# Performance work log

Measured on AMD Instinct MI355X. Metric: run time of the kernel, lower is better.

The kernel has to match this reference:

```python
import jax, jax.numpy as jnp
import numpy as np

N = 8192
IN_F = 256
HEADS = 4
HF = 64            # head_features = out_features / heads
OUT_F = HEADS * HF # concat=True
NEG_SLOPE = 0.2


def setup_inputs() -> dict:
    key = jax.random.key(0)
    ks = jax.random.split(key, 7)
    x = jax.random.normal(ks[0], (N, IN_F), dtype=jnp.float32)
    graph = jax.random.randint(ks[1], (N, N), 0, 2, dtype=jnp.int32)
    weight = jax.random.normal(ks[2], (HEADS, IN_F, HF), dtype=jnp.float32) * (1.0 / np.sqrt(IN_F))
    weight_i = jax.random.normal(ks[3], (HEADS, HF, 1), dtype=jnp.float32) * (1.0 / np.sqrt(HF))
    weight_j = jax.random.normal(ks[4], (HEADS, HF, 1), dtype=jnp.float32) * (1.0 / np.sqrt(HF))
    weight_r = jax.random.normal(ks[5], (IN_F, HF * HEADS), dtype=jnp.float32) * (1.0 / np.sqrt(IN_F))
    bias = jnp.zeros((OUT_F,), dtype=jnp.float32)
    return {"x": x, "graph": graph, "weight": weight, "weight_i": weight_i,
            "weight_j": weight_j, "weight_r": weight_r, "bias": bias}


def reference(x, graph, weight, weight_i, weight_j, weight_r, bias):
    # h: per-head projected features [heads, N, hf]
    h = jnp.einsum('nm,hmf->hnf', x, weight)
    # additive attention logits: coe_i [h,N,1] + coe_j [h,1,N]
    coe_i = jnp.einsum('hnf,hfo->hno', h, weight_i)          # [heads, N, 1]
    coe_j = jnp.einsum('hnf,hfo->hno', h, weight_j)          # [heads, N, 1]
    coe = jax.nn.leaky_relu(coe_i + jnp.swapaxes(coe_j, 1, 2), NEG_SLOPE)  # [heads, N, N]
    # adjacency mask (note transpose, matching the torch code)
    mask = jnp.where(graph > 0, 0.0, -jnp.inf).T             # [N, N]
    att = jax.nn.softmax(coe + mask[None], axis=-1)          # [heads, N, N]
    # aggregate and move heads to axis 1: [N, heads, hf]
    y = jnp.einsum('hij,hjf->ihf', att, h)
    # residual with projection (in_features != head_features)
    y = y + (x @ weight_r).reshape(N, HEADS, HF)
    # concat heads + bias
    y = y.reshape(N, OUT_F) + bias
    return y
```

## Files before the change

### kernel.cpp

```cpp
#include <hip/hip_runtime.h>
#include <hip/hip_bf16.h>

#define N 8192
#define IN_F 256
#define HEADS 4
#define HF 64
#define OUT_F 256

typedef __attribute__((ext_vector_type(8))) short short8;
typedef __attribute__((ext_vector_type(4))) float f32x4;

__device__ __forceinline__ float lrelu(float x) {
    return fmaxf(x, 0.0f) * 0.8f + x * 0.2f;
}
__device__ __forceinline__ short f2bf(float f) {
    union { __hip_bfloat16 h; short s; } u;
    u.h = __float2bfloat16(f);
    return u.s;
}
__device__ __forceinline__ float bf2f(unsigned short b) {
    union { unsigned u; float f; } v; v.u = ((unsigned)b) << 16;
    return v.f;
}
__device__ __forceinline__ unsigned pack_bf16(float p0, float p1) {
    union { __hip_bfloat162 b; unsigned u; } cv;
    cv.b = __float22bfloat162_rn(make_float2(p0, p1));
    return cv.u;
}

__global__ __launch_bounds__(256) void k_wcvt(
    const float* __restrict__ w, const float* __restrict__ wr,
    unsigned short* __restrict__ BbT)
{
    int c = blockIdx.x;
    int k = threadIdx.x;
    float v;
    if (c < 256) {
        int head = c >> 6, f = c & 63;
        v = w[((size_t)head * IN_F + k) * HF + f];
    } else {
        v = wr[(size_t)k * OUT_F + (c - 256)];
    }
    BbT[(size_t)c * IN_F + k] = (unsigned short)f2bf(v);
}

__global__ __launch_bounds__(256) void k_gemm(
    const float* __restrict__ x, const unsigned short* __restrict__ BbT,
    const float* __restrict__ bias,
    unsigned short* __restrict__ hT, float* __restrict__ out)
{
    __shared__ unsigned short Asw[64 * 64];
    __shared__ unsigned short Bsw[128 * 64];
    int t = threadIdx.x;
    int m0 = blockIdx.x * 64;
    int bn = blockIdx.y;
    int w_ = t >> 6, l = t & 63;
    int wr_ = w_ >> 1, wc_ = w_ & 1;
    int ar = l & 15, g = l >> 4;

    f32x4 acc[2][4];
    #pragma unroll
    for (int m = 0; m < 2; ++m)
        #pragma unroll
        for (int n = 0; n < 4; ++n) acc[m][n] = (f32x4){0.f, 0.f, 0.f, 0.f};

    int srow = t >> 2, skq = (t & 3) * 16;
    int sc = t >> 1, sh = (t & 1) * 32;

    for (int kt = 0; kt < 4; ++kt) {
        const float* xs = x + (size_t)(m0 + srow) * IN_F + kt * 64 + skq;
        float4 xa = ((const float4*)xs)[0];
        float4 xb = ((const float4*)xs)[1];
        float4 xc = ((const float4*)xs)[2];
        float4 xd = ((const float4*)xs)[3];
        unsigned ae[8];
        ae[0] = pack_bf16(xa.x, xa.y); ae[1] = pack_bf16(xa.z, xa.w);
        ae[2] = pack_bf16(xb.x, xb.y); ae[3] = pack_bf16(xb.z, xb.w);
        ae[4] = pack_bf16(xc.x, xc.y); ae[5] = pack_bf16(xc.z, xc.w);
        ae[6] = pack_bf16(xd.x, xd.y); ae[7] = pack_bf16(xd.z, xd.w);
        int kb0 = (skq >> 3) ^ (srow & 7);
        int kb1 = ((skq >> 3) + 1) ^ (srow & 7);
        *(uint4*)&Asw[srow * 64 + kb0 * 8] = *(uint4*)&ae[0];
        *(uint4*)&Asw[srow * 64 + kb1 * 8] = *(uint4*)&ae[4];
        const unsigned short* bs = BbT + (size_t)(bn * 128 + sc) * IN_F + kt * 64 + sh;
        uint4 b0 = ((const uint4*)bs)[0];
        uint4 b1 = ((const uint4*)bs)[1];
        uint4 b2 = ((const uint4*)bs)[2];
        uint4 b3 = ((const uint4*)bs)[3];
        int hb = sh >> 3;
        *(uint4*)&Bsw[sc * 64 + ((hb + 0) ^ (sc & 7)) * 8] = b0;
        *(uint4*)&Bsw[sc * 64 + ((hb + 1) ^ (sc & 7)) * 8] = b1;
        *(uint4*)&Bsw[sc * 64 + ((hb + 2) ^ (sc & 7)) * 8] = b2;
        *(uint4*)&Bsw[sc * 64 + ((hb + 3) ^ (sc & 7)) * 8] = b3;
        __syncthreads();
        #pragma unroll
        for (int ks = 0; ks < 2; ++ks) {
            short8 af[2], bf[4];
            #pragma unroll
            for (int m = 0; m < 2; ++m) {
                int row = wr_ * 32 + m * 16 + ar;
                int kb = (ks * 4 + g) ^ (row & 7);
                af[m] = *(const short8*)&Asw[row * 64 + kb * 8];
            }
            #pragma unroll
            for (int n = 0; n < 4; ++n) {
                int c = wc_ * 64 + n * 16 + ar;
                int kb = (ks * 4 + g) ^ (c & 7);
                bf[n] = *(const short8*)&Bsw[c * 64 + kb * 8];
            }
            #pragma unroll
            for (int m = 0; m < 2; ++m)
                #pragma unroll
                for (int n = 0; n < 4; ++n)
                    acc[m][n] = __builtin_amdgcn_mfma_f32_16x16x32_bf16(af[m], bf[n], acc[m][n], 0, 0, 0);
        }
        __syncthreads();
    }
    #pragma unroll
    for (int m = 0; m < 2; ++m) {
        #pragma unroll
        for (int n = 0; n < 4; ++n) {
            int cg = bn * 128 + wc_ * 64 + n * 16 + ar;
            int mg0 = m0 + wr_ * 32 + m * 16 + g * 4;
            if (cg < 256) {
                int head = cg >> 6, f = cg & 63;
                unsigned pk[2];
                pk[0] = pack_bf16(acc[m][n][0], acc[m][n][1]);
                pk[1] = pack_bf16(acc[m][n][2], acc[m][n][3]);
                *(uint2*)(hT + (size_t)(head * HF + f) * N + mg0) = *(uint2*)pk;
            } else {
                float bb = bias[cg - 256];
                #pragma unroll
                for (int r = 0; r < 4; ++r)
                    out[(size_t)(mg0 + r) * OUT_F + (cg - 256)] = acc[m][n][r] + bb;
            }
        }
    }
}

__global__ __launch_bounds__(256) void k_coe(
    const unsigned short* __restrict__ hT, const float* __restrict__ wi,
    const float* __restrict__ wj, float* __restrict__ coe_i, float* __restrict__ coe_j)
{
    int head = blockIdx.y;
    int n = blockIdx.x * 256 + threadIdx.x;
    const unsigned short* hp = hT + (size_t)head * HF * N + n;
    float si = 0.f, sj = 0.f;
    #pragma unroll 8
    for (int f = 0; f < HF; ++f) {
        float hv = bf2f(hp[(size_t)f * N]);
        si = fmaf(hv, wi[head * HF + f], si);
        sj = fmaf(hv, wj[head * HF + f], sj);
    }
    coe_i[head * N + n] = si;
    coe_j[head * N + n] = sj;
}

__global__ __launch_bounds__(256) void k_cols(
    const float* __restrict__ coe_j, float* __restrict__ maxB,
    float* __restrict__ F, float* __restrict__ H)
{
    __shared__ float red[256];
    int head = blockIdx.x;
    int t = threadIdx.x;
    float m = -1e30f;
    for (int n = t; n < N; n += 256) {
        float b = coe_j[head * N + n];
        F[head * N + n] = __expf(b);
        H[head * N + n] = __expf(0.2f * b);
        m = fmaxf(m, b);
    }
    red[t] = m;
    __syncthreads();
    for (int s = 128; s > 0; s >>= 1) {
        if (t < s) red[t] = fmaxf(red[t], red[t + s]);
        __syncthreads();
    }
    if (t == 0) maxB[head] = red[0];
}

__global__ __launch_bounds__(256) void k_pack(
    const int* __restrict__ graph, unsigned int* __restrict__ bits)
{
    int i = blockIdx.y * 256 + threadIdx.x;
    int jw = blockIdx.x;
    const int* gp = graph + (size_t)(jw * 32) * N + i;
    unsigned int word = 0;
    #pragma unroll
    for (int k = 0; k < 32; ++k)
        word |= (gp[(size_t)k * N] > 0 ? 1u : 0u) << k;
    bits[(size_t)jw * N + i] = word;
}

__device__ __forceinline__ short8 makeP(
    const float* __restrict__ Fp, const float* __restrict__ Hp, int jt,
    unsigned int mk, float Ei, float Gi)
{
    float4 fa = *(const float4*)(Fp + jt);
    float4 fb2 = *(const float4*)(Fp + jt + 4);
    float4 ha = *(const float4*)(Hp + jt);
    float4 hb2 = *(const float4*)(Hp + jt + 4);
    float fv[8] = {fa.x, fa.y, fa.z, fa.w, fb2.x, fb2.y, fb2.z, fb2.w};
    float hv[8] = {ha.x, ha.y, ha.z, ha.w, hb2.x, hb2.y, hb2.z, hb2.w};
    union { short8 s8; unsigned u[4]; } A;
    #pragma unroll
    for (int jp = 0; jp < 4; ++jp) {
        float p0 = fmaxf(Ei * fv[2 * jp],     Gi * hv[2 * jp]);
        float p1 = fmaxf(Ei * fv[2 * jp + 1], Gi * hv[2 * jp + 1]);
        int s0 = ((int)(mk << (31 - 2 * jp))) >> 31;
        int s1 = ((int)(mk << (30 - 2 * jp))) >> 31;
        p0 = __int_as_float(__float_as_int(p0) & s0);
        p1 = __int_as_float(__float_as_int(p1) & s1);
        A.u[jp] = pack_bf16(p0, p1);
    }
    return A.s8;
}

__global__ __launch_bounds__(512) void k_att(
    const unsigned short* __restrict__ hT, const float* __restrict__ coe_i,
    const float* __restrict__ maxB, const float* __restrict__ F,
    const float* __restrict__ H, const unsigned int* __restrict__ bits,
    float* __restrict__ out)
{
    __shared__ char smem[32768];
    unsigned short* hb = (unsigned short*)smem;
    float* mbuf = (float*)smem;

    int t = threadIdx.x;
    int head = blockIdx.y;
    int i0 = blockIdx.x * 64;
    int w = t >> 6, l = t & 63;
    int wrow = w & 3, grp = w >> 2;
    int ar = l & 15, g = l >> 4, g8 = g * 8;

    int irow = i0 + wrow * 16 + ar;
    float a = coe_i[head * N + irow];
    float M = lrelu(a + maxB[head]);
    float Ei = __expf(a - M);
    float Gi = __expf(0.2f * a - M);

    f32x4 acc[4];
    #pragma unroll
    for (int fb = 0; fb < 4; ++fb) acc[fb] = (f32x4){0.f, 0.f, 0.f, 0.f};
    f32x4 accd = (f32x4){0.f, 0.f, 0.f, 0.f};

    short8 ones;
    #pragma unroll
    for (int k = 0; k < 8; ++k) ones[k] = (short)0x3F80;

    int sbuf = t >> 8;
    int u = t & 255;
    int sf = u >> 2, sj = (u & 3) * 16;
    const unsigned short* hrow = hT + ((size_t)(head * HF + sf) * N) + sj;
    int pg0 = ((sj >> 3) + 0) ^ (sf & 7);
    int pg1 = ((sj >> 3) + 1) ^ (sf & 7);
    int wo = sbuf * 4096 + sf * 64;

    const float* Fp = F + head * N + g8;
    const float* Hp = H + head * N + g8;
    const unsigned int* bp = bits + irow;

    uint4 hv0 = *(const uint4*)(hrow + sbuf * 64);
    uint4 hv1 = *(const uint4*)(hrow + sbuf * 64 + 8);

    for (int s = 0; s < 64; ++s) {
        int jt = s * 128 + grp * 64;
        size_t jw = (size_t)(jt >> 5);
        unsigned int mk0 = bp[jw * N] >> g8;
        unsigned int mk1 = bp[(jw + 1) * N] >> g8;
        int bo = (s & 1) * 8192;
        *(uint4*)&hb[bo + wo + pg0 * 8] = hv0;
        *(uint4*)&hb[bo + wo + pg1 * 8] = hv1;
        int sn = (s + 1 < 64) ? s + 1 : s;
        hv0 = *(const uint4*)(hrow + sn * 128 + sbuf * 64);
        hv1 = *(const uint4*)(hrow + sn * 128 + sbuf * 64 + 8);

        short8 af0 = makeP(Fp, Hp, jt, mk0, Ei, Gi);
        short8 af1 = makeP(Fp, Hp, jt + 32, mk1, Ei, Gi);

        __syncthreads();

        const unsigned short* rb = &hb[bo + grp * 4096];
        #pragma unroll
        for (int ss = 0; ss < 2; ++ss) {
            short8 af = ss ? af1 : af0;
            #pragma unroll
            for (int fb = 0; fb < 4; ++fb) {
                int row = fb * 16 + ar;
                int pg = (ss * 4 + g) ^ (ar & 7);
                short8 bfr = *(const short8*)&rb[row * 64 + pg * 8];
                acc[fb] = __builtin_amdgcn_mfma_f32_16x16x32_bf16(af, bfr, acc[fb], 0, 0, 0);
            }
            accd = __builtin_amdgcn_mfma_f32_16x16x32_bf16(af, ones, accd, 0, 0, 0);
        }
    }

    __syncthreads();
    int mb = (wrow * 64 + l) * 21;
    if (grp == 1) {
        #pragma unroll
        for (int fb = 0; fb < 4; ++fb)
            #pragma unroll
            for (int r = 0; r < 4; ++r)
                mbuf[mb + fb * 4 + r] = acc[fb][r];
        #pragma unroll
        for (int r = 0; r < 4; ++r)
            mbuf[mb + 16 + r] = accd[r];
    }
    __syncthreads();
    if (grp == 0) {
        #pragma unroll
        for (int fb = 0; fb < 4; ++fb)
            #pragma unroll
            for (int r = 0; r < 4; ++r)
                acc[fb][r] += mbuf[mb + fb * 4 + r];
        #pragma unroll
        for (int r = 0; r < 4; ++r)
            accd[r] += mbuf[mb + 16 + r];
        #pragma unroll
        for (int r = 0; r < 4; ++r) {
            float inv = 1.0f / accd[r];
            int orow = i0 + wrow * 16 + g * 4 + r;
            float* op = out + (size_t)orow * OUT_F + head * HF + ar;
            #pragma unroll
            for (int fb = 0; fb < 4; ++fb)
                op[fb * 16] += acc[fb][r] * inv;
        }
    }
}

extern "C" void kernel_launch(void* const* d_in, const int* in_sizes, int n_in,
                              void* d_out, int out_size, void* d_ws, size_t ws_size,
                              hipStream_t stream) {
    const float* x     = (const float*)d_in[0];
    const int*   graph = (const int*)d_in[1];
    const float* w     = (const float*)d_in[2];
    const float* wi    = (const float*)d_in[3];
    const float* wj    = (const float*)d_in[4];
    const float* wr    = (const float*)d_in[5];
    const float* bias  = (const float*)d_in[6];
    float* out = (float*)d_out;

    char* ws = (char*)d_ws;
    unsigned short* hT  = (unsigned short*)(ws);
    float* coe_i = (float*)(ws + 4194304);
    float* coe_j = (float*)(ws + 4325376);
    float* maxB  = (float*)(ws + 4456448);
    float* F     = (float*)(ws + 4457472);
    float* H     = (float*)(ws + 4588544);
    unsigned short* BbT = (unsigned short*)(ws + 4719616);
    unsigned int* bits  = (unsigned int*)(ws + 4981760);

    k_wcvt<<<dim3(512), 256, 0, stream>>>(w, wr, BbT);
    k_gemm<<<dim3(128, 4), 256, 0, stream>>>(x, BbT, bias, hT, out);
    k_coe<<<dim3(32, 4), 256, 0, stream>>>(hT, wi, wj, coe_i, coe_j);
    k_cols<<<dim3(4), 256, 0, stream>>>(coe_j, maxB, F, H);
    k_pack<<<dim3(256, 32), 256, 0, stream>>>(graph, bits);
    k_att<<<dim3(N / 64, HEADS), 512, 0, stream>>>(hT, coe_i, maxB, F, H, bits, out);
}
```

Before: 178.4 us.

## Give each wave two row tiles and split j across four wave groups

Restructures the attention kernel so each wave computes two 16-row tiles that share the same LDS B-fragments and F/H loads. The j dimension is now split four ways across wave groups, with 256 columns per step, which halves the loop trip count and barrier count. The LDS staging buffer doubles to 64KB, and the final reduction now combines three partial sums through shared memory. The cost is higher register pressure from two accumulator sets and a larger LDS footprint, which may reduce occupancy.

Result: faster. 169.1 us (-5.2%).

```diff
diff --git a/kernel.cpp b/kernel.cpp
--- a/kernel.cpp
+++ b/kernel.cpp
@@ -193,15 +193,11 @@
 }
 
 __device__ __forceinline__ short8 makeP(
-    const float* __restrict__ Fp, const float* __restrict__ Hp, int jt,
+    const float4& fa, const float4& fb4, const float4& ha, const float4& hb4,
     unsigned int mk, float Ei, float Gi)
 {
-    float4 fa = *(const float4*)(Fp + jt);
-    float4 fb2 = *(const float4*)(Fp + jt + 4);
-    float4 ha = *(const float4*)(Hp + jt);
-    float4 hb2 = *(const float4*)(Hp + jt + 4);
-    float fv[8] = {fa.x, fa.y, fa.z, fa.w, fb2.x, fb2.y, fb2.z, fb2.w};
-    float hv[8] = {ha.x, ha.y, ha.z, ha.w, hb2.x, hb2.y, hb2.z, hb2.w};
+    float fv[8] = {fa.x, fa.y, fa.z, fa.w, fb4.x, fb4.y, fb4.z, fb4.w};
+    float hv[8] = {ha.x, ha.y, ha.z, ha.w, hb4.x, hb4.y, hb4.z, hb4.w};
     union { short8 s8; unsigned u[4]; } A;
     #pragma unroll
     for (int jp = 0; jp < 4; ++jp) {
@@ -222,7 +218,7 @@
     const float* __restrict__ H, const unsigned int* __restrict__ bits,
     float* __restrict__ out)
 {
-    __shared__ char smem[32768];
+    __shared__ char smem[65536];
     unsigned short* hb = (unsigned short*)smem;
     float* mbuf = (float*)smem;
 
@@ -230,101 +226,153 @@
     int head = blockIdx.y;
     int i0 = blockIdx.x * 64;
     int w = t >> 6, l = t & 63;
-    int wrow = w & 3, grp = w >> 2;
+    int rg = w >> 2, grp = w & 3;
     int ar = l & 15, g = l >> 4, g8 = g * 8;
 
-    int irow = i0 + wrow * 16 + ar;
-    float a = coe_i[head * N + irow];
-    float M = lrelu(a + maxB[head]);
-    float Ei = __expf(a - M);
-    float Gi = __expf(0.2f * a - M);
-
-    f32x4 acc[4];
-    #pragma unroll
-    for (int fb = 0; fb < 4; ++fb) acc[fb] = (f32x4){0.f, 0.f, 0.f, 0.f};
-    f32x4 accd = (f32x4){0.f, 0.f, 0.f, 0.f};
+    int irow0 = i0 + rg * 32 + ar;
+    int irow1 = irow0 + 16;
+    float mB = maxB[head];
+    float a0 = coe_i[head * N + irow0];
+    float a1 = coe_i[head * N + irow1];
+    float M0 = lrelu(a0 + mB);
+    float M1 = lrelu(a1 + mB);
+    float Ei0 = __expf(a0 - M0), Gi0 = __expf(0.2f * a0 - M0);
+    float Ei1 = __expf(a1 - M1), Gi1 = __expf(0.2f * a1 - M1);
+
+    f32x4 acc0[4], acc1[4];
+    #pragma unroll
+    for (int fb = 0; fb < 4; ++fb) {
+        acc0[fb] = (f32x4){0.f, 0.f, 0.f, 0.f};
+        acc1[fb] = (f32x4){0.f, 0.f, 0.f, 0.f};
+    }
+    f32x4 accd0 = (f32x4){0.f, 0.f, 0.f, 0.f};
+    f32x4 accd1 = (f32x4){0.f, 0.f, 0.f, 0.f};
 
     short8 ones;
     #pragma unroll
     for (int k = 0; k < 8; ++k) ones[k] = (short)0x3F80;
 
-    int sbuf = t >> 8;
-    int u = t & 255;
-    int sf = u >> 2, sj = (u & 3) * 16;
-    const unsigned short* hrow = hT + ((size_t)(head * HF + sf) * N) + sj;
-    int pg0 = ((sj >> 3) + 0) ^ (sf & 7);
-    int pg1 = ((sj >> 3) + 1) ^ (sf & 7);
-    int wo = sbuf * 4096 + sf * 64;
+    int grp_s = t >> 7;
+    int v = t & 127;
+    int sf = v >> 1;
+    int gsel = v & 1;
+    const unsigned short* hsrc = hT + ((size_t)(head * HF + sf) * N) + grp_s * 64 + gsel * 32;
+    int sfk = sf & 7;
+    int wbase = grp_s * 4096 + sf * 64;
+    int pgA = ((gsel * 4 + 0) ^ sfk) * 8;
+    int pgB = ((gsel * 4 + 1) ^ sfk) * 8;
+    int pgC = ((gsel * 4 + 2) ^ sfk) * 8;
+    int pgD = ((gsel * 4 + 3) ^ sfk) * 8;
 
     const float* Fp = F + head * N + g8;
     const float* Hp = H + head * N + g8;
-    const unsigned int* bp = bits + irow;
-
-    uint4 hv0 = *(const uint4*)(hrow + sbuf * 64);
-    uint4 hv1 = *(const uint4*)(hrow + sbuf * 64 + 8);
-
-    for (int s = 0; s < 64; ++s) {
-        int jt = s * 128 + grp * 64;
+    const unsigned int* bp0 = bits + irow0;
+    const unsigned int* bp1 = bits + irow1;
+
+    uint4 hv0 = *(const uint4*)(hsrc + 0);
+    uint4 hv1 = *(const uint4*)(hsrc + 8);
+    uint4 hv2 = *(const uint4*)(hsrc + 16);
+    uint4 hv3 = *(const uint4*)(hsrc + 24);
+
+    for (int s = 0; s < 32; ++s) {
+        int jt = s * 256 + grp * 64;
         size_t jw = (size_t)(jt >> 5);
-        unsigned int mk0 = bp[jw * N] >> g8;
-        unsigned int mk1 = bp[(jw + 1) * N] >> g8;
-        int bo = (s & 1) * 8192;
-        *(uint4*)&hb[bo + wo + pg0 * 8] = hv0;
-        *(uint4*)&hb[bo + wo + pg1 * 8] = hv1;
-        int sn = (s + 1 < 64) ? s + 1 : s;
-        hv0 = *(const uint4*)(hrow + sn * 128 + sbuf * 64);
-        hv1 = *(const uint4*)(hrow + sn * 128 + sbuf * 64 + 8);
-
-        short8 af0 = makeP(Fp, Hp, jt, mk0, Ei, Gi);
-        short8 af1 = makeP(Fp, Hp, jt + 32, mk1, Ei, Gi);
+        unsigned int mk00 = bp0[jw * N] >> g8;
+        unsigned int mk01 = bp0[(jw + 1) * N] >> g8;
+        unsigned int mk10 = bp1[jw * N] >> g8;
+        unsigned int mk11 = bp1[(jw + 1) * N] >> g8;
+        int bo = (s & 1) * 16384;
+        *(uint4*)&hb[bo + wbase + pgA] = hv0;
+        *(uint4*)&hb[bo + wbase + pgB] = hv1;
+        *(uint4*)&hb[bo + wbase + pgC] = hv2;
+        *(uint4*)&hb[bo + wbase + pgD] = hv3;
+        int sn = (s + 1 < 32) ? s + 1 : s;
+        const unsigned short* hn = hsrc + (size_t)sn * 256;
+        hv0 = *(const uint4*)(hn + 0);
+        hv1 = *(const uint4*)(hn + 8);
+        hv2 = *(const uint4*)(hn + 16);
+        hv3 = *(const uint4*)(hn + 24);
+
+        float4 fa0 = *(const float4*)(Fp + jt);
+        float4 fb0 = *(const float4*)(Fp + jt + 4);
+        float4 ha0 = *(const float4*)(Hp + jt);
+        float4 hb0 = *(const float4*)(Hp + jt + 4);
+        short8 af00 = makeP(fa0, fb0, ha0, hb0, mk00, Ei0, Gi0);
+        short8 af10 = makeP(fa0, fb0, ha0, hb0, mk10, Ei1, Gi1);
+        float4 fa1 = *(const float4*)(Fp + jt + 32);
+        float4 fb1 = *(const float4*)(Fp + jt + 36);
+        float4 ha1 = *(const float4*)(Hp + jt + 32);
+        float4 hb1 = *(const float4*)(Hp + jt + 36);
+        short8 af01 = makeP(fa1, fb1, ha1, hb1, mk01, Ei0, Gi0);
+        short8 af11 = makeP(fa1, fb1, ha1, hb1, mk11, Ei1, Gi1);
 
         __syncthreads();
 
         const unsigned short* rb = &hb[bo + grp * 4096];
         #pragma unroll
         for (int ss = 0; ss < 2; ++ss) {
-            short8 af = ss ? af1 : af0;
+            short8 a0f = ss ? af01 : af00;
+            short8 a1f = ss ? af11 : af10;
             #pragma unroll
             for (int fb = 0; fb < 4; ++fb) {
                 int row = fb * 16 + ar;
                 int pg = (ss * 4 + g) ^ (ar & 7);
                 short8 bfr = *(const short8*)&rb[row * 64 + pg * 8];
-                acc[fb] = __builtin_amdgcn_mfma_f32_16x16x32_bf16(af, bfr, acc[fb], 0, 0, 0);
-            }
-            accd = __builtin_amdgcn_mfma_f32_16x16x32_bf16(af, ones, accd, 0, 0, 0);
+                acc0[fb] = __builtin_amdgcn_mfma_f32_16x16x32_bf16(a0f, bfr, acc0[fb], 0, 0, 0);
+                acc1[fb] = __builtin_amdgcn_mfma_f32_16x16x32_bf16(a1f, bfr, acc1[fb], 0, 0, 0);
+            }
+            accd0 = __builtin_amdgcn_mfma_f32_16x16x32_bf16(a0f, ones, accd0, 0, 0, 0);
+            accd1 = __builtin_amdgcn_mfma_f32_16x16x32_bf16(a1f, ones, accd1, 0, 0, 0);
         }
     }
 
     __syncthreads();
-    int mb = (wrow * 64 + l) * 21;
-    if (grp == 1) {
+    int slot = rg * 64 + l;
+    if (grp > 0) {
+        float* dst = mbuf + (size_t)(grp - 1) * 5248 + slot * 41;
         #pragma unroll
         for (int fb = 0; fb < 4; ++fb)
             #pragma unroll
-            for (int r = 0; r < 4; ++r)
-                mbuf[mb + fb * 4 + r] = acc[fb][r];
-        #pragma unroll
-        for (int r = 0; r < 4; ++r)
-            mbuf[mb + 16 + r] = accd[r];
+            for (int r = 0; r < 4; ++r) {
+                dst[fb * 4 + r] = acc0[fb][r];
+                dst[16 + fb * 4 + r] = acc1[fb][r];
+            }
+        #pragma unroll
+        for (int r = 0; r < 4; ++r) {
+            dst[32 + r] = accd0[r];
+            dst[36 + r] = accd1[r];
+        }
     }
     __syncthreads();
     if (grp == 0) {
         #pragma unroll
-        for (int fb = 0; fb < 4; ++fb)
-            #pragma unroll
-            for (int r = 0; r < 4; ++r)
-                acc[fb][r] += mbuf[mb + fb * 4 + r];
-        #pragma unroll
-        for (int r = 0; r < 4; ++r)
-            accd[r] += mbuf[mb + 16 + r];
+        for (int q = 0; q < 3; ++q) {
+            const float* src = mbuf + (size_t)q * 5248 + slot * 41;
+            #pragma unroll
+            for (int fb = 0; fb < 4; ++fb)
+                #pragma unroll
+                for (int r = 0; r < 4; ++r) {
+                    acc0[fb][r] += src[fb * 4 + r];
+                    acc1[fb][r] += src[16 + fb * 4 + r];
+                }
+            #pragma unroll
+            for (int r = 0; r < 4; ++r) {
+                accd0[r] += src[32 + r];
+                accd1[r] += src[36 + r];
+            }
+        }
         #pragma unroll
         for (int r = 0; r < 4; ++r) {
-            float inv = 1.0f / accd[r];
-            int orow = i0 + wrow * 16 + g * 4 + r;
-            float* op = out + (size_t)orow * OUT_F + head * HF + ar;
-            #pragma unroll
-            for (int fb = 0; fb < 4; ++fb)
-                op[fb * 16] += acc[fb][r] * inv;
+            float inv0 = 1.0f / accd0[r];
+            float inv1 = 1.0f / accd1[r];
+            int orow0 = i0 + rg * 32 + g * 4 + r;
+            float* op0 = out + (size_t)orow0 * OUT_F + head * HF + ar;
+            float* op1 = op0 + 16 * OUT_F;
+            #pragma unroll
+            for (int fb = 0; fb < 4; ++fb) {
+                op0[fb * 16] += acc0[fb][r] * inv0;
+                op1[fb * 16] += acc1[fb][r] * inv1;
+            }
         }
     }
 }
```
